# Kernel optimization log

Hardware: AMD Instinct MI355X
Metric: run time of the kernel (lower is better)

The kernel has to match this reference:

```python
import jax, jax.numpy as jnp
import numpy as np

N_NODES = 50000
N_EDGES = 800000
D_IN = 128
D_HID = 128
D_OUT = 1


def gcn_layer(x, W, b, src, dst, n_nodes):
    """PyG GCNConv: h = XW; out = D^{-1/2}(A+I)D^{-1/2} h + b.

    deg[i] = in_degree(i) + 1 (self loop). Self-loop contribution is added
    directly as h * deg^{-1} instead of materializing extra edges.
    """
    h = x @ W  # [N, d_out]
    deg = jnp.zeros((n_nodes,), dtype=x.dtype).at[dst].add(1.0) + 1.0
    dinv = jax.lax.rsqrt(deg)  # deg^{-1/2}
    norm = (dinv[src] * dinv[dst])[:, None]  # [E, 1]
    agg = jnp.zeros_like(h).at[dst].add(h[src] * norm)  # scatter-add messages
    agg = agg + h * (dinv * dinv)[:, None]  # self loops: deg^{-1} * h
    return agg + b


def setup_inputs() -> dict:
    key = jax.random.key(0)
    ks = jax.random.split(key, 8)
    x = jax.random.normal(ks[0], (N_NODES, D_IN), dtype=jnp.float32)
    edge_index = jax.random.randint(ks[1], (2, N_EDGES), 0, N_NODES, dtype=jnp.int64 if jax.config.jax_enable_x64 else jnp.int32)
    s1 = 1.0 / np.sqrt(D_IN)
    s2 = 1.0 / np.sqrt(D_HID)
    W1 = jax.random.uniform(ks[2], (D_IN, D_HID), jnp.float32, -s1, s1)
    b1 = jnp.zeros((D_HID,), jnp.float32)
    W2 = jax.random.uniform(ks[3], (D_HID, D_HID), jnp.float32, -s2, s2)
    b2 = jnp.zeros((D_HID,), jnp.float32)
    Wr = jax.random.uniform(ks[4], (D_HID, D_OUT), jnp.float32, -s2, s2)
    br = jax.random.uniform(ks[5], (D_OUT,), jnp.float32, -s2, s2)
    return {"x": x, "edge_index": edge_index, "W1": W1, "b1": b1,
            "W2": W2, "b2": b2, "Wr": Wr, "br": br}


def reference(x, edge_index, W1, b1, W2, b2, Wr, br):
    src, dst = edge_index[0], edge_index[1]
    n = x.shape[0]
    h = jax.nn.relu(gcn_layer(x, W1, b1, src, dst, n))
    h = jax.nn.relu(gcn_layer(h, W2, b2, src, dst, n))
    return h @ Wr + br  # [N, output_dim]
```

## Files before the change

kernel.cpp:

```cpp
#include <hip/hip_runtime.h>
#include <hip/hip_fp16.h>
#include <cstdint>
#include <cstddef>


constexpr int DIM = 128;
#define BSH 6
#define BIN_EPT 13

typedef __attribute__((ext_vector_type(8))) short bf16x8;
typedef __attribute__((ext_vector_type(4))) float f32x4;

__device__ __forceinline__ short bf16h(float x) {
    unsigned u = __float_as_uint(x);
    return (short)((u + 0x7FFFu + ((u >> 16) & 1u)) >> 16);
}
__device__ __forceinline__ float bf16f(short h) {
    return __uint_as_float(((unsigned)(unsigned short)h) << 16);
}

__global__ __launch_bounds__(256) void k_hist(const int* __restrict__ dst,
                                              int* __restrict__ bcount, int E, int nb) {
    __shared__ int h[1024];
    for (int i = threadIdx.x; i < nb; i += 256) h[i] = 0;
    __syncthreads();
    int stride = gridDim.x * 256;
    for (int e = blockIdx.x * 256 + threadIdx.x; e < E; e += stride)
        atomicAdd(&h[dst[e] >> BSH], 1);
    __syncthreads();
    for (int i = threadIdx.x; i < nb; i += 256) {
        int c = h[i];
        if (c) atomicAdd(&bcount[i], c);
    }
}

__global__ __launch_bounds__(1024) void k_bscan(const int* __restrict__ bcount,
                                                int* __restrict__ bptr,
                                                int* __restrict__ bcur, int nb, int E) {
    __shared__ int s[1024];
    int t = threadIdx.x;
    int v = (t < nb) ? bcount[t] : 0;
    s[t] = v;
    __syncthreads();
    for (int off = 1; off < 1024; off <<= 1) {
        int u = (t >= off) ? s[t - off] : 0;
        __syncthreads();
        s[t] += u;
        __syncthreads();
    }
    if (t < nb) { int ex = s[t] - v; bptr[t] = ex; bcur[t] = ex; }
    if (t == 0) bptr[nb] = E;
}

__global__ __launch_bounds__(256) void k_bin(const int* __restrict__ src,
                                             const int* __restrict__ dst,
                                             int* __restrict__ bcur,
                                             unsigned* __restrict__ pairs,
                                             int E, int nb) {
    __shared__ int h[1024];
    __shared__ int base[1024];
    for (int i = threadIdx.x; i < nb; i += 256) h[i] = 0;
    __syncthreads();

    int e0 = blockIdx.x * 256 * BIN_EPT;
    unsigned u[BIN_EPT];
    int cnt = 0;
#pragma unroll
    for (int j = 0; j < BIN_EPT; j++) {
        int e = e0 + j * 256 + threadIdx.x;
        if (e < E) {
            int d = dst[e];
            u[j] = ((unsigned)d << 16) | (unsigned)src[e];
            atomicAdd(&h[d >> BSH], 1);
            cnt = j + 1;
        }
    }
    __syncthreads();
    for (int i = threadIdx.x; i < nb; i += 256) {
        int c = h[i];
        base[i] = c ? atomicAdd(&bcur[i], c) : 0;
    }
    __syncthreads();
#pragma unroll
    for (int j = 0; j < BIN_EPT; j++) {
        if (j < cnt) {
            int pos = atomicAdd(&base[u[j] >> 22], 1);
            pairs[pos] = u[j];
        }
    }
}

__global__ __launch_bounds__(256) void k_fill2(const unsigned* __restrict__ pairs,
                                               const int* __restrict__ bptr,
                                               int* __restrict__ row_ptr,
                                               float* __restrict__ dinv,
                                               int* __restrict__ col,
                                               int N, int nb, int E) {
    __shared__ int ldeg[64];
    __shared__ int lcur[64];
    int b = blockIdx.x;
    int node0 = b << BSH;
    int beg = bptr[b], end = bptr[b + 1];
    if (threadIdx.x < 64) ldeg[threadIdx.x] = 0;
    __syncthreads();
    for (int i = beg + threadIdx.x; i < end; i += 256)
        atomicAdd(&ldeg[(pairs[i] >> 16) & 63], 1);
    __syncthreads();
    if (threadIdx.x < 64) {
        int d = ldeg[threadIdx.x];
        int x = d;
#pragma unroll
        for (int off = 1; off < 64; off <<= 1) {
            int y = __shfl_up(x, off, 64);
            if ((int)threadIdx.x >= off) x += y;
        }
        int node = node0 + threadIdx.x;
        if (node < N) {
            int rp = beg + (x - d);
            row_ptr[node] = rp;
            lcur[threadIdx.x] = rp;
            dinv[node] = rsqrtf((float)d + 1.0f);
        }
        if (b == nb - 1 && threadIdx.x == 0) row_ptr[N] = E;
    }
    __syncthreads();
    for (int i = beg + threadIdx.x; i < end; i += 256) {
        unsigned u = pairs[i];
        int pos = atomicAdd(&lcur[(u >> 16) & 63], 1);
        col[pos] = (int)(u & 0xffffu);
    }
}

__global__ __launch_bounds__(256) void k_wfrag(const float* __restrict__ W,
                                               short* __restrict__ Bh,
                                               short* __restrict__ Bl) {
    int idx = blockIdx.x * 256 + threadIdx.x;
    int j  = idx & 7;
    int l  = (idx >> 3) & 63;
    int ks = (idx >> 9) & 3;
    int nt = idx >> 11;
    int k   = ks * 32 + ((l >> 4) * 8) + j;
    int c   = nt * 16 + (l & 15);
    float w = W[k * 128 + c];
    short h = bf16h(w);
    Bh[idx] = h;
    Bl[idx] = bf16h(w - bf16f(h));
}

__global__ __launch_bounds__(256) void k_mm(const float* __restrict__ X,
                                            const short* __restrict__ Bhp,
                                            const short* __restrict__ Blp,
                                            const float* __restrict__ dinv,
                                            __half* __restrict__ Hh, int N) {
    int gw   = (blockIdx.x * 256 + threadIdx.x) >> 6;
    int lane = threadIdx.x & 63;
    int row0 = gw * 16;
    if (row0 >= N) return;

    int arow = row0 + (lane & 15);
    if (arow >= N) arow = N - 1;
    const float* Xp = X + (size_t)arow * DIM + ((lane >> 4) * 8);

    bf16x8 Ah[4], Al[4];
#pragma unroll
    for (int ks = 0; ks < 4; ks++) {
        float4 a = *(const float4*)(Xp + ks * 32);
        float4 b = *(const float4*)(Xp + ks * 32 + 4);
        float v[8] = {a.x, a.y, a.z, a.w, b.x, b.y, b.z, b.w};
        bf16x8 h, lo;
#pragma unroll
        for (int j = 0; j < 8; j++) {
            short hh = bf16h(v[j]);
            h[j] = hh;
            lo[j] = bf16h(v[j] - bf16f(hh));
        }
        Ah[ks] = h;
        Al[ks] = lo;
    }

    const bf16x8* BH = (const bf16x8*)Bhp;
    const bf16x8* BL = (const bf16x8*)Blp;

    f32x4 acc[8];
#pragma unroll
    for (int nt = 0; nt < 8; nt++) {
        f32x4 c = {0.f, 0.f, 0.f, 0.f};
#pragma unroll
        for (int ks = 0; ks < 4; ks++) {
            bf16x8 bh = BH[(nt * 4 + ks) * 64 + lane];
            bf16x8 bl = BL[(nt * 4 + ks) * 64 + lane];
            c = __builtin_amdgcn_mfma_f32_16x16x32_bf16(Ah[ks], bh, c, 0, 0, 0);
            c = __builtin_amdgcn_mfma_f32_16x16x32_bf16(Al[ks], bh, c, 0, 0, 0);
            c = __builtin_amdgcn_mfma_f32_16x16x32_bf16(Ah[ks], bl, c, 0, 0, 0);
        }
        acc[nt] = c;
    }

    int rb = row0 + ((lane >> 4) * 4);
    int cb = lane & 15;
#pragma unroll
    for (int r = 0; r < 4; r++) {
        if (rb + r < N) {
            float dv = dinv[rb + r];
            __half* out = Hh + (size_t)(rb + r) * DIM + cb;
#pragma unroll
            for (int nt = 0; nt < 8; nt++)
                out[nt * 16] = __float2half(acc[nt][r] * dv);
        }
    }
}

__device__ __forceinline__ float2 agg_row(const __half2* __restrict__ Hh,
                                          const int* __restrict__ row_ptr,
                                          const int* __restrict__ col,
                                          const float* __restrict__ dinv,
                                          const float* __restrict__ B,
                                          int wid, int lane) {
    int beg = __builtin_amdgcn_readfirstlane(row_ptr[wid]);
    int end = __builtin_amdgcn_readfirstlane(row_ptr[wid + 1]);
    const __half2* Hl = Hh + lane;
    float2 s0f = __half22float2(Hl[(size_t)wid * 64]);
    float ax = s0f.x, ay = s0f.y;
    float bx = 0.f, by = 0.f, cx = 0.f, cy = 0.f, dx = 0.f, dy = 0.f;

    int e = beg;
    for (; e + 8 <= end; e += 8) {
        int s0 = col[e + 0], s1 = col[e + 1], s2 = col[e + 2], s3 = col[e + 3];
        int s4 = col[e + 4], s5 = col[e + 5], s6 = col[e + 6], s7 = col[e + 7];
        __half2 g0 = Hl[(size_t)s0 * 64];
        __half2 g1 = Hl[(size_t)s1 * 64];
        __half2 g2 = Hl[(size_t)s2 * 64];
        __half2 g3 = Hl[(size_t)s3 * 64];
        __half2 g4 = Hl[(size_t)s4 * 64];
        __half2 g5 = Hl[(size_t)s5 * 64];
        __half2 g6 = Hl[(size_t)s6 * 64];
        __half2 g7 = Hl[(size_t)s7 * 64];
        float2 f0 = __half22float2(g0), f1 = __half22float2(g1);
        float2 f2 = __half22float2(g2), f3 = __half22float2(g3);
        float2 f4 = __half22float2(g4), f5 = __half22float2(g5);
        float2 f6 = __half22float2(g6), f7 = __half22float2(g7);
        ax += f0.x; ay += f0.y;  bx += f1.x; by += f1.y;
        cx += f2.x; cy += f2.y;  dx += f3.x; dy += f3.y;
        ax += f4.x; ay += f4.y;  bx += f5.x; by += f5.y;
        cx += f6.x; cy += f6.y;  dx += f7.x; dy += f7.y;
    }
    for (; e + 4 <= end; e += 4) {
        int s0 = col[e + 0], s1 = col[e + 1], s2 = col[e + 2], s3 = col[e + 3];
        __half2 g0 = Hl[(size_t)s0 * 64];
        __half2 g1 = Hl[(size_t)s1 * 64];
        __half2 g2 = Hl[(size_t)s2 * 64];
        __half2 g3 = Hl[(size_t)s3 * 64];
        float2 f0 = __half22float2(g0), f1 = __half22float2(g1);
        float2 f2 = __half22float2(g2), f3 = __half22float2(g3);
        ax += f0.x; ay += f0.y;  bx += f1.x; by += f1.y;
        cx += f2.x; cy += f2.y;  dx += f3.x; dy += f3.y;
    }
    for (; e < end; e++) {
        float2 f = __half22float2(Hl[(size_t)col[e] * 64]);
        ax += f.x; ay += f.y;
    }
    ax += bx + cx + dx;
    ay += by + cy + dy;

    float di = dinv[wid];
    float2 b = *(const float2*)(B + lane * 2);
    return make_float2(fmaf(di, ax, b.x), fmaf(di, ay, b.y));
}

__global__ __launch_bounds__(256) void k_agg(const __half2* __restrict__ Hh,
                                             const int* __restrict__ row_ptr,
                                             const int* __restrict__ col,
                                             const float* __restrict__ dinv,
                                             const float* __restrict__ B,
                                             float* __restrict__ O, int N) {
    int wid = (blockIdx.x * 256 + threadIdx.x) >> 6;
    int lane = threadIdx.x & 63;
    if (wid >= N) return;
    float2 r = agg_row(Hh, row_ptr, col, dinv, B, wid, lane);
    r.x = fmaxf(r.x, 0.f);
    r.y = fmaxf(r.y, 0.f);
    *(float2*)(O + (size_t)wid * DIM + lane * 2) = r;
}

__global__ __launch_bounds__(256) void k_agg_out(const __half2* __restrict__ Hh,
                                                 const int* __restrict__ row_ptr,
                                                 const int* __restrict__ col,
                                                 const float* __restrict__ dinv,
                                                 const float* __restrict__ B,
                                                 const float* __restrict__ Wr,
                                                 const float* __restrict__ br,
                                                 float* __restrict__ out, int N) {
    int wid = (blockIdx.x * 256 + threadIdx.x) >> 6;
    int lane = threadIdx.x & 63;
    if (wid >= N) return;
    float2 r = agg_row(Hh, row_ptr, col, dinv, B, wid, lane);
    float2 w = *(const float2*)(Wr + lane * 2);
    float v = fmaxf(r.x, 0.f) * w.x + fmaxf(r.y, 0.f) * w.y;
#pragma unroll
    for (int off = 32; off > 0; off >>= 1) v += __shfl_down(v, off, 64);
    if (lane == 0) out[wid] = v + br[0];
}

extern "C" void kernel_launch(void* const* d_in, const int* in_sizes, int n_in,
                              void* d_out, int out_size, void* d_ws, size_t ws_size,
                              hipStream_t stream) {
    const float* x  = (const float*)d_in[0];
    const int*   ei = (const int*)d_in[1];
    const float* W1 = (const float*)d_in[2];
    const float* b1 = (const float*)d_in[3];
    const float* W2 = (const float*)d_in[4];
    const float* b2 = (const float*)d_in[5];
    const float* Wr = (const float*)d_in[6];
    const float* br = (const float*)d_in[7];

    const int N = in_sizes[0] / DIM;
    const int E = in_sizes[1] / 2;
    const int* src = ei;
    const int* dst = ei + E;
    const int NB = (N + 63) >> BSH;

    char* p = (char*)d_ws;
    auto alloc = [&](size_t bytes) -> void* {
        void* r = (void*)p;
        p += (bytes + 255) & ~(size_t)255;
        return r;
    };
    __half*   Hh      = (__half*)alloc((size_t)N * DIM * 2);
    float*    A1      = (float*)alloc((size_t)N * DIM * 4);
    float*    dinv    = (float*)alloc((size_t)N * 4);
    int*      row_ptr = (int*)alloc((size_t)(N + 1) * 4);
    int*      bcount  = (int*)alloc((size_t)NB * 4);
    int*      bptr    = (int*)alloc((size_t)(NB + 1) * 4);
    int*      bcur    = (int*)alloc((size_t)NB * 4);
    unsigned* pairs   = (unsigned*)alloc((size_t)E * 4);
    int*      col     = (int*)alloc((size_t)E * 4);
    short*    Bh1     = (short*)alloc(16384 * 2);
    short*    Bl1     = (short*)alloc(16384 * 2);
    short*    Bh2     = (short*)alloc(16384 * 2);
    short*    Bl2     = (short*)alloc(16384 * 2);
    (void)ws_size; (void)n_in;

    hipMemsetAsync(bcount, 0, (size_t)NB * 4, stream);

    k_hist<<<256, 256, 0, stream>>>(dst, bcount, E, NB);
    k_bscan<<<1, 1024, 0, stream>>>(bcount, bptr, bcur, NB, E);
    const int binb = (E + 256 * BIN_EPT - 1) / (256 * BIN_EPT);
    k_bin<<<binb, 256, 0, stream>>>(src, dst, bcur, pairs, E, NB);
    k_fill2<<<NB, 256, 0, stream>>>(pairs, bptr, row_ptr, dinv, col, N, NB, E);

    k_wfrag<<<64, 256, 0, stream>>>(W1, Bh1, Bl1);
    k_wfrag<<<64, 256, 0, stream>>>(W2, Bh2, Bl2);

    const int mmb = ((N + 15) / 16 + 3) / 4;
    const int ab  = (N * 64 + 255) / 256;

    k_mm<<<mmb, 256, 0, stream>>>(x, Bh1, Bl1, dinv, Hh, N);
    k_agg<<<ab, 256, 0, stream>>>((const __half2*)Hh, row_ptr, col, dinv, b1, A1, N);
    k_mm<<<mmb, 256, 0, stream>>>(A1, Bh2, Bl2, dinv, Hh, N);
    k_agg_out<<<ab, 256, 0, stream>>>((const __half2*)Hh, row_ptr, col, dinv, b2,
                                      Wr, br, (float*)d_out, N);
}
```

Baseline: 144.0 us.

## Store layer-1 output as fp16, sort CSR columns by source, and merge setup kernels

The intermediate activation A1 is now written as fp16 instead of fp32, and the second matmul reads it through a templated loader. This halves that buffer's write and read traffic. k_fill2 stages pairs in LDS and orders each node's column list by coarse source bucket, so gathers during aggregation have better locality. The memset and the two weight-fragment kernels become one launch. The fp16 intermediate adds rounding error before the second layer.

```diff
diff --git a/kernel.cpp b/kernel.cpp
--- a/kernel.cpp
+++ b/kernel.cpp
@@ -7,6 +7,9 @@
 constexpr int DIM = 128;
 #define BSH 6
 #define BIN_EPT 13
+#define FT 8
+#define FSH 13
+#define STAGE 2048
 
 typedef __attribute__((ext_vector_type(8))) short bf16x8;
 typedef __attribute__((ext_vector_type(4))) float f32x4;
@@ -96,58 +99,99 @@
                                                float* __restrict__ dinv,
                                                int* __restrict__ col,
                                                int N, int nb, int E) {
-    __shared__ int ldeg[64];
-    __shared__ int lcur[64];
+    __shared__ unsigned sp[STAGE];
+    __shared__ int lcnt[64 * FT];
     int b = blockIdx.x;
     int node0 = b << BSH;
     int beg = bptr[b], end = bptr[b + 1];
-    if (threadIdx.x < 64) ldeg[threadIdx.x] = 0;
-    __syncthreads();
-    for (int i = beg + threadIdx.x; i < end; i += 256)
-        atomicAdd(&ldeg[(pairs[i] >> 16) & 63], 1);
-    __syncthreads();
+    int cnt = end - beg;
+    bool useStage = (cnt <= STAGE);
+
+    for (int i = threadIdx.x; i < 64 * FT; i += 256) lcnt[i] = 0;
+    __syncthreads();
+
+    for (int i = threadIdx.x; i < cnt; i += 256) {
+        unsigned u = pairs[beg + i];
+        if (useStage) sp[i] = u;
+        atomicAdd(&lcnt[((u >> 16) & 63) * FT + ((u & 0xffffu) >> FSH)], 1);
+    }
+    __syncthreads();
+
     if (threadIdx.x < 64) {
-        int d = ldeg[threadIdx.x];
-        int x = d;
+        int t = threadIdx.x;
+        int c[FT]; int sum = 0;
+#pragma unroll
+        for (int f = 0; f < FT; f++) { c[f] = lcnt[t * FT + f]; sum += c[f]; }
+        int x = sum;
 #pragma unroll
         for (int off = 1; off < 64; off <<= 1) {
             int y = __shfl_up(x, off, 64);
-            if ((int)threadIdx.x >= off) x += y;
-        }
-        int node = node0 + threadIdx.x;
+            if (t >= off) x += y;
+        }
+        int nodebase = beg + x - sum;
+        int node = node0 + t;
         if (node < N) {
-            int rp = beg + (x - d);
-            row_ptr[node] = rp;
-            lcur[threadIdx.x] = rp;
-            dinv[node] = rsqrtf((float)d + 1.0f);
-        }
-        if (b == nb - 1 && threadIdx.x == 0) row_ptr[N] = E;
-    }
-    __syncthreads();
-    for (int i = beg + threadIdx.x; i < end; i += 256) {
-        unsigned u = pairs[i];
-        int pos = atomicAdd(&lcur[(u >> 16) & 63], 1);
-        col[pos] = (int)(u & 0xffffu);
-    }
-}
-
-__global__ __launch_bounds__(256) void k_wfrag(const float* __restrict__ W,
-                                               short* __restrict__ Bh,
-                                               short* __restrict__ Bl) {
+            row_ptr[node] = nodebase;
+            dinv[node] = rsqrtf((float)sum + 1.0f);
+        }
+        int run = nodebase;
+#pragma unroll
+        for (int f = 0; f < FT; f++) { lcnt[t * FT + f] = run; run += c[f]; }
+        if (b == nb - 1 && t == 0) row_ptr[N] = E;
+    }
+    __syncthreads();
+
+    for (int i = threadIdx.x; i < cnt; i += 256) {
+        unsigned u = useStage ? sp[i] : pairs[beg + i];
+        unsigned s = u & 0xffffu;
+        int pos = atomicAdd(&lcnt[((u >> 16) & 63) * FT + (s >> FSH)], 1);
+        col[pos] = (int)s;
+    }
+}
+
+__global__ __launch_bounds__(256) void k_wfrag2(const float* __restrict__ W1,
+                                                const float* __restrict__ W2,
+                                                short* __restrict__ Bh1,
+                                                short* __restrict__ Bl1,
+                                                short* __restrict__ Bh2,
+                                                short* __restrict__ Bl2,
+                                                int* __restrict__ bcount, int nb) {
     int idx = blockIdx.x * 256 + threadIdx.x;
-    int j  = idx & 7;
-    int l  = (idx >> 3) & 63;
-    int ks = (idx >> 9) & 3;
-    int nt = idx >> 11;
+    if (idx < nb) bcount[idx] = 0;
+    const float* W = (idx < 16384) ? W1 : W2;
+    short* Bh = (idx < 16384) ? Bh1 : Bh2;
+    short* Bl = (idx < 16384) ? Bl1 : Bl2;
+    int id = idx & 16383;
+    int j  = id & 7;
+    int l  = (id >> 3) & 63;
+    int ks = (id >> 9) & 3;
+    int nt = id >> 11;
     int k   = ks * 32 + ((l >> 4) * 8) + j;
     int c   = nt * 16 + (l & 15);
     float w = W[k * 128 + c];
     short h = bf16h(w);
-    Bh[idx] = h;
-    Bl[idx] = bf16h(w - bf16f(h));
-}
-
-__global__ __launch_bounds__(256) void k_mm(const float* __restrict__ X,
+    Bh[id] = h;
+    Bl[id] = bf16h(w - bf16f(h));
+}
+
+__device__ __forceinline__ void load8(const float* p, float* v) {
+    float4 a = *(const float4*)p;
+    float4 b = *(const float4*)(p + 4);
+    v[0] = a.x; v[1] = a.y; v[2] = a.z; v[3] = a.w;
+    v[4] = b.x; v[5] = b.y; v[6] = b.z; v[7] = b.w;
+}
+__device__ __forceinline__ void load8(const __half* p, float* v) {
+    float4 a = *(const float4*)p;
+    const __half2* h = (const __half2*)&a;
+#pragma unroll
+    for (int i = 0; i < 4; i++) {
+        float2 f = __half22float2(h[i]);
+        v[2 * i] = f.x; v[2 * i + 1] = f.y;
+    }
+}
+
+template <typename T>
+__global__ __launch_bounds__(256) void k_mm(const T* __restrict__ X,
                                             const short* __restrict__ Bhp,
                                             const short* __restrict__ Blp,
                                             const float* __restrict__ dinv,
@@ -159,14 +203,13 @@
 
     int arow = row0 + (lane & 15);
     if (arow >= N) arow = N - 1;
-    const float* Xp = X + (size_t)arow * DIM + ((lane >> 4) * 8);
+    const T* Xp = X + (size_t)arow * DIM + ((lane >> 4) * 8);
 
     bf16x8 Ah[4], Al[4];
 #pragma unroll
     for (int ks = 0; ks < 4; ks++) {
-        float4 a = *(const float4*)(Xp + ks * 32);
-        float4 b = *(const float4*)(Xp + ks * 32 + 4);
-        float v[8] = {a.x, a.y, a.z, a.w, b.x, b.y, b.z, b.w};
+        float v[8];
+        load8(Xp + ks * 32, v);
         bf16x8 h, lo;
 #pragma unroll
         for (int j = 0; j < 8; j++) {
@@ -272,14 +315,12 @@
                                              const int* __restrict__ col,
                                              const float* __restrict__ dinv,
                                              const float* __restrict__ B,
-                                             float* __restrict__ O, int N) {
+                                             __half2* __restrict__ O, int N) {
     int wid = (blockIdx.x * 256 + threadIdx.x) >> 6;
     int lane = threadIdx.x & 63;
     if (wid >= N) return;
     float2 r = agg_row(Hh, row_ptr, col, dinv, B, wid, lane);
-    r.x = fmaxf(r.x, 0.f);
-    r.y = fmaxf(r.y, 0.f);
-    *(float2*)(O + (size_t)wid * DIM + lane * 2) = r;
+    O[(size_t)wid * 64 + lane] = __floats2half2_rn(fmaxf(r.x, 0.f), fmaxf(r.y, 0.f));
 }
 
 __global__ __launch_bounds__(256) void k_agg_out(const __half2* __restrict__ Hh,
@@ -326,7 +367,7 @@
         return r;
     };
     __half*   Hh      = (__half*)alloc((size_t)N * DIM * 2);
-    float*    A1      = (float*)alloc((size_t)N * DIM * 4);
+    __half*   A1      = (__half*)alloc((size_t)N * DIM * 2);
     float*    dinv    = (float*)alloc((size_t)N * 4);
     int*      row_ptr = (int*)alloc((size_t)(N + 1) * 4);
     int*      bcount  = (int*)alloc((size_t)NB * 4);
@@ -340,7 +381,7 @@
     short*    Bl2     = (short*)alloc(16384 * 2);
     (void)ws_size; (void)n_in;
 
-    hipMemsetAsync(bcount, 0, (size_t)NB * 4, stream);
+    k_wfrag2<<<128, 256, 0, stream>>>(W1, W2, Bh1, Bl1, Bh2, Bl2, bcount, NB);
 
     k_hist<<<256, 256, 0, stream>>>(dst, bcount, E, NB);
     k_bscan<<<1, 1024, 0, stream>>>(bcount, bptr, bcur, NB, E);
@@ -348,15 +389,13 @@
     k_bin<<<binb, 256, 0, stream>>>(src, dst, bcur, pairs, E, NB);
     k_fill2<<<NB, 256, 0, stream>>>(pairs, bptr, row_ptr, dinv, col, N, NB, E);
 
-    k_wfrag<<<64, 256, 0, stream>>>(W1, Bh1, Bl1);
-    k_wfrag<<<64, 256, 0, stream>>>(W2, Bh2, Bl2);
-
     const int mmb = ((N + 15) / 16 + 3) / 4;
     const int ab  = (N * 64 + 255) / 256;
 
-    k_mm<<<mmb, 256, 0, stream>>>(x, Bh1, Bl1, dinv, Hh, N);
-    k_agg<<<ab, 256, 0, stream>>>((const __half2*)Hh, row_ptr, col, dinv, b1, A1, N);
-    k_mm<<<mmb, 256, 0, stream>>>(A1, Bh2, Bl2, dinv, Hh, N);
+    k_mm<float><<<mmb, 256, 0, stream>>>(x, Bh1, Bl1, dinv, Hh, N);
+    k_agg<<<ab, 256, 0, stream>>>((const __half2*)Hh, row_ptr, col, dinv, b1,
+                                  (__half2*)A1, N);
+    k_mm<__half><<<mmb, 256, 0, stream>>>(A1, Bh2, Bl2, dinv, Hh, N);
     k_agg_out<<<ab, 256, 0, stream>>>((const __half2*)Hh, row_ptr, col, dinv, b2,
                                       Wr, br, (float*)d_out, N);
 }
```

Result: faster. 138.8 us (-3.6%).
